# Optimization experiments

Measured on AMD Instinct MI355X. Metric: run time of the kernel, lower is better.

## Reference

```python
import jax, jax.numpy as jnp
import numpy as np

N_HEAD = 16

def setup_inputs() -> dict:
    key = jax.random.key(0)
    k1, k2, k3 = jax.random.split(key, 3)
    B, T, C = 2, 2048, 1024
    x_norm_for_qk = jax.random.normal(k1, (B, T, C), dtype=jnp.float32)
    xt_current_for_v = jax.random.normal(k2, (B, T, C), dtype=jnp.float32)
    W_attn = jax.random.normal(k3, (C, 2 * C), dtype=jnp.float32) * (1.0 / np.sqrt(C))
    b_attn = jnp.zeros((2 * C,), dtype=jnp.float32)
    return {"x_norm_for_qk": x_norm_for_qk, "xt_current_for_v": xt_current_for_v,
            "W_attn": W_attn, "b_attn": b_attn}

def reference(x_norm_for_qk, xt_current_for_v, W_attn, b_attn):
    B, T, C = x_norm_for_qk.shape
    H = N_HEAD
    D = C // H  # head dim
    qk = x_norm_for_qk @ W_attn + b_attn          # [B,T,2C]
    q, k = qk[..., :C], qk[..., C:]
    q = q.reshape(B, T, H, D).transpose(0, 2, 1, 3)   # [B,H,T,D]
    k = k.reshape(B, T, H, D).transpose(0, 2, 1, 3)
    v = xt_current_for_v.reshape(B, T, H, D).transpose(0, 2, 1, 3)
    scale = 1.0 / np.sqrt(D).astype(np.float32)
    scores = jnp.einsum('bhqd,bhkd->bhqk', q, k) * scale  # [B,H,T,T]
    causal = jnp.tril(jnp.ones((T, T), dtype=bool))
    scores = jnp.where(causal[None, None], scores, jnp.float32(-jnp.inf))
    weights = jax.nn.softmax(scores, axis=-1)  # dropout p=0.0 -> identity
    y = jnp.einsum('bhqk,bhkd->bhqd', weights, v)
    return y.transpose(0, 2, 1, 3).reshape(B, T, C)
```

## Files before the change

### kernel.cpp

```cpp
#include <hip/hip_runtime.h>
#include <hip/hip_bf16.h>
#include <math.h>

typedef __attribute__((ext_vector_type(8))) short s8v;
typedef __attribute__((ext_vector_type(4))) float f4v;
typedef __attribute__((ext_vector_type(16))) float f16v;
typedef __attribute__((ext_vector_type(2))) unsigned int u32x2;
typedef unsigned short ush;
typedef unsigned int u32;

#define QSCALE 0.180336880f
#define FIXED_M 10.0f

static __device__ __forceinline__ ush f2bf(float f) {
    u32 x = __builtin_bit_cast(u32, f);
    return (ush)((x + 0x7fffu + ((x >> 16) & 1u)) >> 16);
}
static __device__ __forceinline__ u32 bfpack(float lo, float hi) {
    u32 a = __builtin_bit_cast(u32, lo) + 0x8000u;
    u32 b = __builtin_bit_cast(u32, hi) + 0x8000u;
    return __builtin_amdgcn_perm(b, a, 0x07060302);
}
static __device__ __forceinline__ u32 cvtpk(float lo, float hi) {
    u32 r;
    asm("v_cvt_pk_bf16_f32 %0, %1, %2" : "=v"(r) : "v"(lo), "v"(hi));
    return r;
}
static __device__ __forceinline__ void gl_lds16(const void* g, void* l) {
    __builtin_amdgcn_global_load_lds(
        (const __attribute__((address_space(1))) u32*)g,
        (__attribute__((address_space(3))) u32*)l, 16, 0, 0);
}
#if __has_builtin(__builtin_amdgcn_exp2f)
#define EXP2F(x) __builtin_amdgcn_exp2f(x)
#else
#define EXP2F(x) exp2f(x)
#endif

static __device__ __forceinline__ void pl32swap(u32& a, u32& b) {
#if __has_builtin(__builtin_amdgcn_permlane32_swap)
    u32x2 r = __builtin_amdgcn_permlane32_swap(a, b, false, false);
    a = r[0]; b = r[1];
#else
    asm volatile("v_permlane32_swap_b32 %0, %1" : "+v"(a), "+v"(b));
#endif
}
static __device__ __forceinline__ s8v mkfrag(u32 a, u32 b, u32 c, u32 d) {
    union { u32 w[4]; s8v v; } u;
    u.w[0] = a; u.w[1] = b; u.w[2] = c; u.w[3] = d;
    return u.v;
}

static __device__ __forceinline__ void softpack(
    const f16v& s0, const f16v& s1, bool needmask, int kbase, int qg,
    float& lrp, s8v& pf0, s8v& pf1, s8v& pf2, s8v& pf3)
{
    float ps = 0.f;
    u32 w0[4], w1[4], x0[4], x1[4];
    if (needmask) {
        #pragma unroll
        for (int g4 = 0; g4 < 4; ++g4) {
            const int kb0 = kbase + 8 * g4;
            float e0a = (kb0 + 0 > qg) ? 0.f : EXP2F(s0[g4 * 4 + 0] - FIXED_M);
            float e0b = (kb0 + 1 > qg) ? 0.f : EXP2F(s0[g4 * 4 + 1] - FIXED_M);
            float e0c = (kb0 + 2 > qg) ? 0.f : EXP2F(s0[g4 * 4 + 2] - FIXED_M);
            float e0d = (kb0 + 3 > qg) ? 0.f : EXP2F(s0[g4 * 4 + 3] - FIXED_M);
            float e1a = (kb0 + 32 > qg) ? 0.f : EXP2F(s1[g4 * 4 + 0] - FIXED_M);
            float e1b = (kb0 + 33 > qg) ? 0.f : EXP2F(s1[g4 * 4 + 1] - FIXED_M);
            float e1c = (kb0 + 34 > qg) ? 0.f : EXP2F(s1[g4 * 4 + 2] - FIXED_M);
            float e1d = (kb0 + 35 > qg) ? 0.f : EXP2F(s1[g4 * 4 + 3] - FIXED_M);
            ps += (e0a + e0b) + (e0c + e0d) + (e1a + e1b) + (e1c + e1d);
            w0[g4] = cvtpk(e0a, e0b); w1[g4] = cvtpk(e0c, e0d);
            x0[g4] = cvtpk(e1a, e1b); x1[g4] = cvtpk(e1c, e1d);
        }
    } else {
        #pragma unroll
        for (int g4 = 0; g4 < 4; ++g4) {
            float e0a = EXP2F(s0[g4 * 4 + 0] - FIXED_M);
            float e0b = EXP2F(s0[g4 * 4 + 1] - FIXED_M);
            float e0c = EXP2F(s0[g4 * 4 + 2] - FIXED_M);
            float e0d = EXP2F(s0[g4 * 4 + 3] - FIXED_M);
            float e1a = EXP2F(s1[g4 * 4 + 0] - FIXED_M);
            float e1b = EXP2F(s1[g4 * 4 + 1] - FIXED_M);
            float e1c = EXP2F(s1[g4 * 4 + 2] - FIXED_M);
            float e1d = EXP2F(s1[g4 * 4 + 3] - FIXED_M);
            ps += (e0a + e0b) + (e0c + e0d) + (e1a + e1b) + (e1c + e1d);
            w0[g4] = cvtpk(e0a, e0b); w1[g4] = cvtpk(e0c, e0d);
            x0[g4] = cvtpk(e1a, e1b); x1[g4] = cvtpk(e1c, e1d);
        }
    }
    lrp += ps;
    pl32swap(w0[0], w0[1]); pl32swap(w1[0], w1[1]);
    pl32swap(w0[2], w0[3]); pl32swap(w1[2], w1[3]);
    pl32swap(x0[0], x0[1]); pl32swap(x1[0], x1[1]);
    pl32swap(x0[2], x0[3]); pl32swap(x1[2], x1[3]);
    pf0 = mkfrag(w0[0], w1[0], w0[1], w1[1]);
    pf1 = mkfrag(w0[2], w1[2], w0[3], w1[3]);
    pf2 = mkfrag(x0[0], x1[0], x0[1], x1[1]);
    pf3 = mkfrag(x0[2], x1[2], x0[3], x1[3]);
}

__global__ __launch_bounds__(256) void prep_kernel(
    const float* __restrict__ X, const float* __restrict__ W,
    const float* __restrict__ XV,
    ush* __restrict__ Xb, ush* __restrict__ Wt, ush* __restrict__ Vtb)
{
    __shared__ float Ts[64][68];
    const int tid = threadIdx.x;
    const int bid = blockIdx.x;
    if (bid < 2048) {
        const size_t i = ((size_t)bid * 256 + tid) * 8;
        float4 v0 = *(const float4*)(X + i);
        float4 v1 = *(const float4*)(X + i + 4);
        uint4 o;
        o.x = bfpack(v0.x, v0.y); o.y = bfpack(v0.z, v0.w);
        o.z = bfpack(v1.x, v1.y); o.w = bfpack(v1.z, v1.w);
        *(uint4*)(Xb + i) = o;
    } else if (bid < 2560) {
        const int id = bid - 2048;
        const int n0 = (id & 31) * 64, k0 = (id >> 5) * 64;
        #pragma unroll
        for (int p = 0; p < 4; ++p) {
            const int idx = p * 256 + tid;
            const int kr = idx >> 4, nc4 = idx & 15;
            float4 v = *(const float4*)(W + (size_t)(k0 + kr) * 2048 + n0 + nc4 * 4);
            Ts[kr][nc4 * 4 + 0] = v.x; Ts[kr][nc4 * 4 + 1] = v.y;
            Ts[kr][nc4 * 4 + 2] = v.z; Ts[kr][nc4 * 4 + 3] = v.w;
        }
        __syncthreads();
        const int n = tid >> 2, kb = (tid & 3) * 16;
        #pragma unroll
        for (int p = 0; p < 4; ++p) {
            const int k = kb + p * 4;
            ushort4 o;
            o.x = f2bf(Ts[k + 0][n]); o.y = f2bf(Ts[k + 1][n]);
            o.z = f2bf(Ts[k + 2][n]); o.w = f2bf(Ts[k + 3][n]);
            *(ushort4*)(Wt + (size_t)(n0 + n) * 1024 + k0 + k) = o;
        }
    } else {
        const int id = bid - 2560;
        const int t0 = (id & 31) * 64;
        const int bh = id >> 5;
        const int b = bh >> 4, h = bh & 15;
        #pragma unroll
        for (int p = 0; p < 4; ++p) {
            const int idx = p * 256 + tid;
            const int tr = idx >> 4, dc4 = idx & 15;
            float4 v = *(const float4*)(XV + (size_t)(b * 2048 + t0 + tr) * 1024
                                        + h * 64 + dc4 * 4);
            Ts[tr][dc4 * 4 + 0] = v.x; Ts[tr][dc4 * 4 + 1] = v.y;
            Ts[tr][dc4 * 4 + 2] = v.z; Ts[tr][dc4 * 4 + 3] = v.w;
        }
        __syncthreads();
        const int d = tid >> 2, tb = (tid & 3) * 16;
        #pragma unroll
        for (int p = 0; p < 4; ++p) {
            const int tq = tb + p * 4;
            ushort4 o;
            o.x = f2bf(Ts[tq + 0][d]); o.y = f2bf(Ts[tq + 1][d]);
            o.z = f2bf(Ts[tq + 2][d]); o.w = f2bf(Ts[tq + 3][d]);
            *(ushort4*)(Vtb + (size_t)((b * 16 + h) * 64 + d) * 2048 + t0 + tq) = o;
        }
    }
}

__global__ __launch_bounds__(256, 2) void gemm_kernel(
    const ush* __restrict__ Xb, const ush* __restrict__ Wt,
    const float* __restrict__ bias,
    ush* __restrict__ Qb, ush* __restrict__ Kb)
{
    __shared__ ush As[4][128 * 32];
    __shared__ ush Bs[4][128 * 32];

    const int tid = threadIdx.x;
    const int wid = tid >> 6, lane = tid & 63;
    const int quad = lane >> 4, l15 = lane & 15;
    const int wm = wid >> 1, wn = wid & 1;
    const int m0 = blockIdx.y * 128, n0 = blockIdx.x * 128;

    const int lrow = lane >> 2;
    const int lkk = (lane & 3) * 8;
    const size_t arow = (size_t)(m0 + wid * 32 + lrow);
    const size_t brow = (size_t)(n0 + wid * 32 + lrow);

    auto stage = [&](int k) {
        const int k0 = k * 32, sl = k & 3;
        gl_lds16(Xb + arow * 1024 + k0 + lkk, &As[sl][wid * 1024]);
        gl_lds16(Xb + (arow + 16) * 1024 + k0 + lkk, &As[sl][wid * 1024 + 512]);
        gl_lds16(Wt + brow * 1024 + k0 + lkk, &Bs[sl][wid * 1024]);
        gl_lds16(Wt + (brow + 16) * 1024 + k0 + lkk, &Bs[sl][wid * 1024 + 512]);
    };

    f4v acc[4][4];
    #pragma unroll
    for (int i = 0; i < 4; ++i)
        #pragma unroll
        for (int j = 0; j < 4; ++j) acc[i][j] = (f4v){0.f, 0.f, 0.f, 0.f};

    stage(0); stage(1);
    asm volatile("s_waitcnt vmcnt(4)" ::: "memory");
    __builtin_amdgcn_s_barrier();
    __builtin_amdgcn_sched_barrier(0);

    for (int k = 0; k < 32; ++k) {
        const int sl = k & 3;
        const bool pf = (k + 2 < 32);

        s8v a[4], bf[4];
        #pragma unroll
        for (int i = 0; i < 4; ++i)
            a[i] = *(const s8v*)&As[sl][(wm * 64 + i * 16 + l15) * 32 + quad * 8];
        #pragma unroll
        for (int j = 0; j < 4; ++j)
            bf[j] = *(const s8v*)&Bs[sl][(wn * 64 + j * 16 + l15) * 32 + quad * 8];
        __builtin_amdgcn_sched_barrier(0);

        if (pf) stage(k + 2);

        __builtin_amdgcn_s_setprio(1);
        #pragma unroll
        for (int i = 0; i < 4; ++i)
            #pragma unroll
            for (int j = 0; j < 4; ++j)
                acc[i][j] = __builtin_amdgcn_mfma_f32_16x16x32_bf16(
                    a[i], bf[j], acc[i][j], 0, 0, 0);
        __builtin_amdgcn_s_setprio(0);

        if (pf) asm volatile("s_waitcnt vmcnt(4)" ::: "memory");
        else    asm volatile("s_waitcnt vmcnt(0)" ::: "memory");
        __builtin_amdgcn_s_barrier();
        __builtin_amdgcn_sched_barrier(0);
    }

    #pragma unroll
    for (int j = 0; j < 4; ++j) {
        const int n = n0 + wn * 64 + j * 16 + l15;
        const float bv = bias[n];
        const bool is_k = n >= 1024;
        const int nn = n & 1023;
        const int h = nn >> 6, d = nn & 63;
        ush* dst = is_k ? Kb : Qb;
        #pragma unroll
        for (int i = 0; i < 4; ++i) {
            const int mrow = m0 + wm * 64 + i * 16 + quad * 4;
            #pragma unroll
            for (int r = 0; r < 4; ++r) {
                const int m = mrow + r;
                const int b = m >> 11, t = m & 2047;
                float val = acc[i][j][r] + bv;
                if (!is_k) val *= QSCALE;
                dst[(size_t)((b * 16 + h) * 2048 + t) * 64 + d] = f2bf(val);
            }
        }
    }
}

__global__ __launch_bounds__(256, 2) void attn_kernel(
    const ush* __restrict__ Qb, const ush* __restrict__ Kb,
    const ush* __restrict__ Vt, float* __restrict__ Y)
{
    __shared__ ush SMEM[32768];
    ush* Kbuf = SMEM;
    ush* Vbuf = SMEM + 16384;

    const int tid = threadIdx.x;
    const int w = tid >> 6, lane = tid & 63;
    const int l31 = lane & 31, hi = lane >> 5;

    const int idx = blockIdx.x;
    const int half = idx >> 8, pair = idx & 255;
    const int qt = half ? (pair & 15) : 15 - (pair & 15);
    const int bh = (pair >> 4) + half * 16;
    const int b = bh >> 4, h = bh & 15;
    const int q0 = qt * 128;
    const int ktmax = 2 * qt + 1;

    const ush* Qg = Qb + (size_t)bh * 2048 * 64;
    const ush* Kg = Kb + (size_t)bh * 2048 * 64;
    const ush* Vg = Vt + (size_t)bh * 64 * 2048;

    ush* Pw = SMEM + w * 2304;
    {
        const int r8q = lane >> 3, c8 = lane & 7;
        #pragma unroll
        for (int p = 0; p < 4; ++p) {
            const int row = p * 8 + r8q;
            uint4 v = *(const uint4*)(Qg + (size_t)(q0 + w * 32 + row) * 64 + c8 * 8);
            *(uint4*)&Pw[row * 72 + c8 * 8] = v;
        }
    }
    s8v bq[4];
    #pragma unroll
    for (int s = 0; s < 4; ++s)
        bq[s] = *(const s8v*)&Pw[l31 * 72 + s * 16 + hi * 8];
    __syncthreads();

    const int r8 = lane >> 3;
    const int g8 = ((lane & 7) ^ r8) * 8;
    auto stage = [&](int kt) {
        const int buf = kt & 3;
        const int k0e = kt * 64;
        const ush* kg = Kg + (size_t)(k0e + w * 16 + r8) * 64 + g8;
        gl_lds16(kg, &Kbuf[buf * 4096 + (w * 16) * 64]);
        gl_lds16(kg + 8 * 64, &Kbuf[buf * 4096 + (w * 16 + 8) * 64]);
        const ush* vg = Vg + (size_t)(w * 16 + r8) * 2048 + k0e + g8;
        gl_lds16(vg, &Vbuf[buf * 4096 + (w * 16) * 64]);
        gl_lds16(vg + 8 * 2048, &Vbuf[buf * 4096 + (w * 16 + 8) * 64]);
    };

    f16v acco0 = {}, acco1 = {};
    float lrp = 0.f;
    const int qg = q0 + w * 32 + l31;
    const int qwmax = q0 + w * 32 + 31;

    stage(0); stage(1);
    asm volatile("s_waitcnt vmcnt(4)" ::: "memory");
    __builtin_amdgcn_s_barrier();
    __builtin_amdgcn_sched_barrier(0);

    for (int kt = 0; kt <= ktmax; ++kt) {
        const int sl = (kt & 3) * 4096;
        const bool active = (kt * 64) <= qwmax;
        const bool pf = (kt + 2 <= ktmax);

        s8v ak0[4], ak1[4], av0[4], av1[4];
        if (active) {
            #pragma unroll
            for (int s = 0; s < 4; ++s) {
                const int ch = (s << 1) + hi;
                const int row0 = l31, row1 = 32 + l31;
                ak0[s] = *(const s8v*)&Kbuf[sl + row0 * 64 + ((ch ^ (row0 & 7)) << 3)];
                ak1[s] = *(const s8v*)&Kbuf[sl + row1 * 64 + ((ch ^ (row1 & 7)) << 3)];
                av0[s] = *(const s8v*)&Vbuf[sl + row0 * 64 + ((ch ^ (row0 & 7)) << 3)];
                av1[s] = *(const s8v*)&Vbuf[sl + row1 * 64 + ((ch ^ (row1 & 7)) << 3)];
            }
        }
        __builtin_amdgcn_sched_barrier(0);

        if (pf) stage(kt + 2);

        if (active) {
            f16v s0 = {}, s1 = {};
            #pragma unroll
            for (int s = 0; s < 4; ++s) {
                s0 = __builtin_amdgcn_mfma_f32_32x32x16_bf16(ak0[s], bq[s], s0, 0, 0, 0);
                s1 = __builtin_amdgcn_mfma_f32_32x32x16_bf16(ak1[s], bq[s], s1, 0, 0, 0);
            }

            s8v pf0, pf1, pf2, pf3;
            softpack(s0, s1, (kt * 64 + 63) > (q0 + w * 32),
                     kt * 64 + 4 * hi, qg, lrp, pf0, pf1, pf2, pf3);

            acco0 = __builtin_amdgcn_mfma_f32_32x32x16_bf16(av0[0], pf0, acco0, 0, 0, 0);
            acco1 = __builtin_amdgcn_mfma_f32_32x32x16_bf16(av1[0], pf0, acco1, 0, 0, 0);
            acco0 = __builtin_amdgcn_mfma_f32_32x32x16_bf16(av0[1], pf1, acco0, 0, 0, 0);
            acco1 = __builtin_amdgcn_mfma_f32_32x32x16_bf16(av1[1], pf1, acco1, 0, 0, 0);
            acco0 = __builtin_amdgcn_mfma_f32_32x32x16_bf16(av0[2], pf2, acco0, 0, 0, 0);
            acco1 = __builtin_amdgcn_mfma_f32_32x32x16_bf16(av1[2], pf2, acco1, 0, 0, 0);
            acco0 = __builtin_amdgcn_mfma_f32_32x32x16_bf16(av0[3], pf3, acco0, 0, 0, 0);
            acco1 = __builtin_amdgcn_mfma_f32_32x32x16_bf16(av1[3], pf3, acco1, 0, 0, 0);
        }

        if (pf) asm volatile("s_waitcnt vmcnt(4)" ::: "memory");
        else    asm volatile("s_waitcnt vmcnt(0)" ::: "memory");
        __builtin_amdgcn_s_barrier();
        __builtin_amdgcn_sched_barrier(0);
    }

    const float lr = lrp + __shfl_xor(lrp, 32);
    float* LTw = (float*)SMEM + w * (32 * 68);
    const float inv = 1.0f / lr;
    #pragma unroll
    for (int r = 0; r < 16; ++r) {
        const int d = (r & 3) + 8 * (r >> 2) + 4 * hi;
        LTw[l31 * 68 + d] = acco0[r] * inv;
        LTw[l31 * 68 + 32 + d] = acco1[r] * inv;
    }
    const int qr4 = lane >> 4, chk = lane & 15;
    #pragma unroll
    for (int p = 0; p < 8; ++p) {
        const int qrow = p * 4 + qr4;
        f4v v = *(const f4v*)&LTw[qrow * 68 + chk * 4];
        *(float4*)(Y + (size_t)(b * 2048 + q0 + w * 32 + qrow) * 1024
                   + h * 64 + chk * 4) = (float4){v[0], v[1], v[2], v[3]};
    }
}

extern "C" void kernel_launch(void* const* d_in, const int* in_sizes, int n_in,
                              void* d_out, int out_size, void* d_ws,
                              size_t ws_size, hipStream_t stream)
{
    const float* x_qk = (const float*)d_in[0];
    const float* x_v  = (const float*)d_in[1];
    const float* W    = (const float*)d_in[2];
    const float* bias = (const float*)d_in[3];
    float* out = (float*)d_out;

    unsigned char* ws = (unsigned char*)d_ws;
    ush* Xb = (ush*)(ws);
    ush* Wt = (ush*)(ws + (8u << 20));
    ush* Qb = (ush*)(ws + (12u << 20));
    ush* Kb = (ush*)(ws + (20u << 20));
    ush* Vt = (ush*)(ws + (28u << 20));

    prep_kernel<<<3584, 256, 0, stream>>>(x_qk, W, x_v, Xb, Wt, Vt);
    gemm_kernel<<<dim3(16, 32), 256, 0, stream>>>(Xb, Wt, bias, Qb, Kb);
    attn_kernel<<<512, 256, 0, stream>>>(Qb, Kb, Vt, out);
}
```

Baseline: 143.8 us.

## Split attention work across waves by query half and key half

Each wave used to own 32 query rows against all 64 keys of a tile. Now waves form a 2x2 grid: each wave handles 64 query rows against one 32-key half. Partial numerators and row sums from the two key halves are then reduced through shared memory before normalisation. The aim is to halve per-wave K/V LDS fragment loads and to skip fully masked key halves on the diagonal more finely. In exchange it needs more accumulator registers, an extra epilogue reduction with barriers, and more Q fragments held per wave.

```diff
diff --git a/kernel.cpp b/kernel.cpp
--- a/kernel.cpp
+++ b/kernel.cpp
@@ -51,12 +51,12 @@
     return u.v;
 }
 
-static __device__ __forceinline__ void softpack(
-    const f16v& s0, const f16v& s1, bool needmask, int kbase, int qg,
-    float& lrp, s8v& pf0, s8v& pf1, s8v& pf2, s8v& pf3)
+static __device__ __forceinline__ void softpack32(
+    const f16v& s0, bool needmask, int kbase, int qg,
+    float& lrp, s8v& pfa, s8v& pfb)
 {
     float ps = 0.f;
-    u32 w0[4], w1[4], x0[4], x1[4];
+    u32 w0[4], w1[4];
     if (needmask) {
         #pragma unroll
         for (int g4 = 0; g4 < 4; ++g4) {
@@ -65,13 +65,8 @@
             float e0b = (kb0 + 1 > qg) ? 0.f : EXP2F(s0[g4 * 4 + 1] - FIXED_M);
             float e0c = (kb0 + 2 > qg) ? 0.f : EXP2F(s0[g4 * 4 + 2] - FIXED_M);
             float e0d = (kb0 + 3 > qg) ? 0.f : EXP2F(s0[g4 * 4 + 3] - FIXED_M);
-            float e1a = (kb0 + 32 > qg) ? 0.f : EXP2F(s1[g4 * 4 + 0] - FIXED_M);
-            float e1b = (kb0 + 33 > qg) ? 0.f : EXP2F(s1[g4 * 4 + 1] - FIXED_M);
-            float e1c = (kb0 + 34 > qg) ? 0.f : EXP2F(s1[g4 * 4 + 2] - FIXED_M);
-            float e1d = (kb0 + 35 > qg) ? 0.f : EXP2F(s1[g4 * 4 + 3] - FIXED_M);
-            ps += (e0a + e0b) + (e0c + e0d) + (e1a + e1b) + (e1c + e1d);
+            ps += (e0a + e0b) + (e0c + e0d);
             w0[g4] = cvtpk(e0a, e0b); w1[g4] = cvtpk(e0c, e0d);
-            x0[g4] = cvtpk(e1a, e1b); x1[g4] = cvtpk(e1c, e1d);
         }
     } else {
         #pragma unroll
@@ -80,24 +75,15 @@
             float e0b = EXP2F(s0[g4 * 4 + 1] - FIXED_M);
             float e0c = EXP2F(s0[g4 * 4 + 2] - FIXED_M);
             float e0d = EXP2F(s0[g4 * 4 + 3] - FIXED_M);
-            float e1a = EXP2F(s1[g4 * 4 + 0] - FIXED_M);
-            float e1b = EXP2F(s1[g4 * 4 + 1] - FIXED_M);
-            float e1c = EXP2F(s1[g4 * 4 + 2] - FIXED_M);
-            float e1d = EXP2F(s1[g4 * 4 + 3] - FIXED_M);
-            ps += (e0a + e0b) + (e0c + e0d) + (e1a + e1b) + (e1c + e1d);
+            ps += (e0a + e0b) + (e0c + e0d);
             w0[g4] = cvtpk(e0a, e0b); w1[g4] = cvtpk(e0c, e0d);
-            x0[g4] = cvtpk(e1a, e1b); x1[g4] = cvtpk(e1c, e1d);
         }
     }
     lrp += ps;
     pl32swap(w0[0], w0[1]); pl32swap(w1[0], w1[1]);
     pl32swap(w0[2], w0[3]); pl32swap(w1[2], w1[3]);
-    pl32swap(x0[0], x0[1]); pl32swap(x1[0], x1[1]);
-    pl32swap(x0[2], x0[3]); pl32swap(x1[2], x1[3]);
-    pf0 = mkfrag(w0[0], w1[0], w0[1], w1[1]);
-    pf1 = mkfrag(w0[2], w1[2], w0[3], w1[3]);
-    pf2 = mkfrag(x0[0], x1[0], x0[1], x1[1]);
-    pf3 = mkfrag(x0[2], x1[2], x0[3], x1[3]);
+    pfa = mkfrag(w0[0], w1[0], w0[1], w1[1]);
+    pfb = mkfrag(w0[2], w1[2], w0[3], w1[3]);
 }
 
 __global__ __launch_bounds__(256) void prep_kernel(
@@ -266,6 +252,7 @@
     const int tid = threadIdx.x;
     const int w = tid >> 6, lane = tid & 63;
     const int l31 = lane & 31, hi = lane >> 5;
+    const int qh = w >> 1, kh = w & 1;
 
     const int idx = blockIdx.x;
     const int half = idx >> 8, pair = idx & 255;
@@ -289,10 +276,17 @@
             *(uint4*)&Pw[row * 72 + c8 * 8] = v;
         }
     }
-    s8v bq[4];
-    #pragma unroll
-    for (int s = 0; s < 4; ++s)
-        bq[s] = *(const s8v*)&Pw[l31 * 72 + s * 16 + hi * 8];
+    __syncthreads();
+    s8v bq0[4], bq1[4];
+    {
+        const ush* P0 = SMEM + (qh * 2 + 0) * 2304 + l31 * 72;
+        const ush* P1 = SMEM + (qh * 2 + 1) * 2304 + l31 * 72;
+        #pragma unroll
+        for (int s = 0; s < 4; ++s) {
+            bq0[s] = *(const s8v*)&P0[s * 16 + hi * 8];
+            bq1[s] = *(const s8v*)&P1[s * 16 + hi * 8];
+        }
+    }
     __syncthreads();
 
     const int r8 = lane >> 3;
@@ -308,10 +302,11 @@
         gl_lds16(vg + 8 * 2048, &Vbuf[buf * 4096 + (w * 16 + 8) * 64]);
     };
 
-    f16v acco0 = {}, acco1 = {};
-    float lrp = 0.f;
-    const int qg = q0 + w * 32 + l31;
-    const int qwmax = q0 + w * 32 + 31;
+    f16v a00 = {}, a01 = {}, a10 = {}, a11 = {};
+    float lrp0 = 0.f, lrp1 = 0.f;
+    const int qbase = q0 + qh * 64;
+    const int qg0 = qbase + l31;
+    const int qg1 = qbase + 32 + l31;
 
     stage(0); stage(1);
     asm volatile("s_waitcnt vmcnt(4)" ::: "memory");
@@ -320,45 +315,60 @@
 
     for (int kt = 0; kt <= ktmax; ++kt) {
         const int sl = (kt & 3) * 4096;
-        const bool active = (kt * 64) <= qwmax;
+        const int keysmin = kt * 64 + kh * 32;
+        const bool act0 = keysmin <= qbase + 31;
+        const bool act1 = keysmin <= qbase + 63;
         const bool pf = (kt + 2 <= ktmax);
 
-        s8v ak0[4], ak1[4], av0[4], av1[4];
-        if (active) {
+        s8v ak[4], av0[2], av1[2];
+        if (act1) {
+            const int krow = kh * 32 + l31;
             #pragma unroll
             for (int s = 0; s < 4; ++s) {
                 const int ch = (s << 1) + hi;
-                const int row0 = l31, row1 = 32 + l31;
-                ak0[s] = *(const s8v*)&Kbuf[sl + row0 * 64 + ((ch ^ (row0 & 7)) << 3)];
-                ak1[s] = *(const s8v*)&Kbuf[sl + row1 * 64 + ((ch ^ (row1 & 7)) << 3)];
-                av0[s] = *(const s8v*)&Vbuf[sl + row0 * 64 + ((ch ^ (row0 & 7)) << 3)];
-                av1[s] = *(const s8v*)&Vbuf[sl + row1 * 64 + ((ch ^ (row1 & 7)) << 3)];
+                ak[s] = *(const s8v*)&Kbuf[sl + krow * 64 + ((ch ^ (krow & 7)) << 3)];
             }
+            const int r0 = l31, r1 = 32 + l31;
+            #pragma unroll
+            for (int s = 0; s < 2; ++s) {
+                const int ch = kh * 4 + (s << 1) + hi;
+                av0[s] = *(const s8v*)&Vbuf[sl + r0 * 64 + ((ch ^ (r0 & 7)) << 3)];
+                av1[s] = *(const s8v*)&Vbuf[sl + r1 * 64 + ((ch ^ (r1 & 7)) << 3)];
+            }
         }
         __builtin_amdgcn_sched_barrier(0);
 
         if (pf) stage(kt + 2);
 
-        if (active) {
-            f16v s0 = {}, s1 = {};
-            #pragma unroll
-            for (int s = 0; s < 4; ++s) {
-                s0 = __builtin_amdgcn_mfma_f32_32x32x16_bf16(ak0[s], bq[s], s0, 0, 0, 0);
-                s1 = __builtin_amdgcn_mfma_f32_32x32x16_bf16(ak1[s], bq[s], s1, 0, 0, 0);
+        if (act1) {
+            const int kbase = keysmin + 4 * hi;
+            const bool mask0 = (keysmin + 31) > qbase;
+            const bool mask1 = (keysmin + 31) > (qbase + 32);
+
+            if (act0) {
+                f16v s0 = {};
+                #pragma unroll
+                for (int s = 0; s < 4; ++s)
+                    s0 = __builtin_amdgcn_mfma_f32_32x32x16_bf16(ak[s], bq0[s], s0, 0, 0, 0);
+                s8v pfa, pfb;
+                softpack32(s0, mask0, kbase, qg0, lrp0, pfa, pfb);
+                a00 = __builtin_amdgcn_mfma_f32_32x32x16_bf16(av0[0], pfa, a00, 0, 0, 0);
+                a01 = __builtin_amdgcn_mfma_f32_32x32x16_bf16(av1[0], pfa, a01, 0, 0, 0);
+                a00 = __builtin_amdgcn_mfma_f32_32x32x16_bf16(av0[1], pfb, a00, 0, 0, 0);
+                a01 = __builtin_amdgcn_mfma_f32_32x32x16_bf16(av1[1], pfb, a01, 0, 0, 0);
             }
-
-            s8v pf0, pf1, pf2, pf3;
-            softpack(s0, s1, (kt * 64 + 63) > (q0 + w * 32),
-                     kt * 64 + 4 * hi, qg, lrp, pf0, pf1, pf2, pf3);
-
-            acco0 = __builtin_amdgcn_mfma_f32_32x32x16_bf16(av0[0], pf0, acco0, 0, 0, 0);
-            acco1 = __builtin_amdgcn_mfma_f32_32x32x16_bf16(av1[0], pf0, acco1, 0, 0, 0);
-            acco0 = __builtin_amdgcn_mfma_f32_32x32x16_bf16(av0[1], pf1, acco0, 0, 0, 0);
-            acco1 = __builtin_amdgcn_mfma_f32_32x32x16_bf16(av1[1], pf1, acco1, 0, 0, 0);
-            acco0 = __builtin_amdgcn_mfma_f32_32x32x16_bf16(av0[2], pf2, acco0, 0, 0, 0);
-            acco1 = __builtin_amdgcn_mfma_f32_32x32x16_bf16(av1[2], pf2, acco1, 0, 0, 0);
-            acco0 = __builtin_amdgcn_mfma_f32_32x32x16_bf16(av0[3], pf3, acco0, 0, 0, 0);
-            acco1 = __builtin_amdgcn_mfma_f32_32x32x16_bf16(av1[3], pf3, acco1, 0, 0, 0);
+            {
+                f16v s1 = {};
+                #pragma unroll
+                for (int s = 0; s < 4; ++s)
+                    s1 = __builtin_amdgcn_mfma_f32_32x32x16_bf16(ak[s], bq1[s], s1, 0, 0, 0);
+                s8v pfa, pfb;
+                softpack32(s1, mask1, kbase, qg1, lrp1, pfa, pfb);
+                a10 = __builtin_amdgcn_mfma_f32_32x32x16_bf16(av0[0], pfa, a10, 0, 0, 0);
+                a11 = __builtin_amdgcn_mfma_f32_32x32x16_bf16(av1[0], pfa, a11, 0, 0, 0);
+                a10 = __builtin_amdgcn_mfma_f32_32x32x16_bf16(av0[1], pfb, a10, 0, 0, 0);
+                a11 = __builtin_amdgcn_mfma_f32_32x32x16_bf16(av1[1], pfb, a11, 0, 0, 0);
+            }
         }
 
         if (pf) asm volatile("s_waitcnt vmcnt(4)" ::: "memory");
@@ -367,21 +377,46 @@
         __builtin_amdgcn_sched_barrier(0);
     }
 
-    const float lr = lrp + __shfl_xor(lrp, 32);
-    float* LTw = (float*)SMEM + w * (32 * 68);
-    const float inv = 1.0f / lr;
-    #pragma unroll
-    for (int r = 0; r < 16; ++r) {
-        const int d = (r & 3) + 8 * (r >> 2) + 4 * hi;
-        LTw[l31 * 68 + d] = acco0[r] * inv;
-        LTw[l31 * 68 + 32 + d] = acco1[r] * inv;
-    }
+    const float lq0 = lrp0 + __shfl_xor(lrp0, 32);
+    const float lq1 = lrp1 + __shfl_xor(lrp1, 32);
+    float* LTq = (float*)SMEM + qh * (64 * 68);
+    float* Lx = (float*)SMEM + 2 * (64 * 68);
+
+    if (kh == 1) {
+        #pragma unroll
+        for (int r = 0; r < 16; ++r) {
+            const int d = (r & 3) + 8 * (r >> 2) + 4 * hi;
+            LTq[l31 * 68 + d] = a00[r];
+            LTq[l31 * 68 + 32 + d] = a01[r];
+            LTq[(32 + l31) * 68 + d] = a10[r];
+            LTq[(32 + l31) * 68 + 32 + d] = a11[r];
+        }
+        if (hi == 0) {
+            Lx[qh * 64 + l31] = lq0;
+            Lx[qh * 64 + 32 + l31] = lq1;
+        }
+    }
+    __syncthreads();
+    if (kh == 0) {
+        const float li0 = 1.0f / (lq0 + Lx[qh * 64 + l31]);
+        const float li1 = 1.0f / (lq1 + Lx[qh * 64 + 32 + l31]);
+        #pragma unroll
+        for (int r = 0; r < 16; ++r) {
+            const int d = (r & 3) + 8 * (r >> 2) + 4 * hi;
+            LTq[l31 * 68 + d] = (a00[r] + LTq[l31 * 68 + d]) * li0;
+            LTq[l31 * 68 + 32 + d] = (a01[r] + LTq[l31 * 68 + 32 + d]) * li0;
+            LTq[(32 + l31) * 68 + d] = (a10[r] + LTq[(32 + l31) * 68 + d]) * li1;
+            LTq[(32 + l31) * 68 + 32 + d] = (a11[r] + LTq[(32 + l31) * 68 + 32 + d]) * li1;
+        }
+    }
+    __syncthreads();
     const int qr4 = lane >> 4, chk = lane & 15;
     #pragma unroll
     for (int p = 0; p < 8; ++p) {
-        const int qrow = p * 4 + qr4;
-        f4v v = *(const f4v*)&LTw[qrow * 68 + chk * 4];
-        *(float4*)(Y + (size_t)(b * 2048 + q0 + w * 32 + qrow) * 1024
+        const int qrow = w * 32 + p * 4 + qr4;
+        const float* LTs = (float*)SMEM + (qrow >> 6) * (64 * 68);
+        f4v v = *(const f4v*)&LTs[(qrow & 63) * 68 + chk * 4];
+        *(float4*)(Y + (size_t)(b * 2048 + q0 + qrow) * 1024
                    + h * 64 + chk * 4) = (float4){v[0], v[1], v[2], v[3]};
     }
 }
```

Result: no change. 143.3 us (-0.3%).
